# Kernel optimization log

Measured on AMD Instinct MI355X. Metric: run time of the kernel, lower is better.

The kernel has to match this reference:

```python
import jax, jax.numpy as jnp
import numpy as np


def _diffuse(x, A):
    # x: [B,C,N,L], A: [B,V,W] -> out[b,c,v,l] = sum_w x[b,c,w,l] * A[b,v,w]
    return jnp.einsum('ncwl,nvw->ncvl', x, A)


def setup_inputs() -> dict:
    key = jax.random.key(0)
    kx, k0, k1, k2, kw = jax.random.split(key, 5)
    B, C, N, L = 32, 40, 512, 12
    C_OUT = 20
    C_CAT = 7 * C  # (order*support_len + 1) * c_in = (2*3+1)*40
    x = jax.random.normal(kx, (B, C, N, L), dtype=jnp.float32)
    def mk_support(k):
        a = jax.random.uniform(k, (B, N, N), dtype=jnp.float32)
        return a / jnp.sum(a, axis=-1, keepdims=True)  # row-normalized transition
    A0, A1, A2 = mk_support(k0), mk_support(k1), mk_support(k2)
    # Conv2d(c_cat, c_out, kernel=(1,2), dilation=2) weights, stored [c_out, c_cat, 2]
    W = jax.random.normal(kw, (C_OUT, C_CAT, 2), dtype=jnp.float32) * 0.05
    b = jnp.zeros((C_OUT,), dtype=jnp.float32)
    return {'x': x, 'A0': A0, 'A1': A1, 'A2': A2, 'W': W, 'b': b}


def reference(x, A0, A1, A2, W, b):
    # dgcn.forward (eval mode, dropout is identity): order=2, support_len=3
    out = [x]
    for A in (A0, A1, A2):
        x1 = _diffuse(x, A)
        out.append(x1)
        x2 = _diffuse(x1, A)
        out.append(x2)
    h = jnp.concatenate(out, axis=1)  # [B, 7C, N, L]
    # linear_: Conv2d kernel (1,2), dilation 2, no padding -> taps at t and t+2, L_out = L-2
    y = (jnp.einsum('ncvl,oc->novl', h[..., :-2], W[:, :, 0])
         + jnp.einsum('ncvl,oc->novl', h[..., 2:], W[:, :, 1])
         + b[None, :, None, None])
    return y
```

## Files before the change

kernel.cpp:

```cpp
#include <hip/hip_runtime.h>
#include <hip/hip_bf16.h>


typedef unsigned short u16;
typedef u16 u16x4 __attribute__((ext_vector_type(4)));
typedef u16 u16x8 __attribute__((ext_vector_type(8)));
typedef __bf16 bf16x8 __attribute__((ext_vector_type(8)));
typedef float f32x4 __attribute__((ext_vector_type(4)));

#define GLD_LDS16(g, l)  __builtin_amdgcn_global_load_lds( \
    (const __attribute__((address_space(1))) void*)(g),    \
    (__attribute__((address_space(3))) void*)(l), 16, 0, 0)

__device__ __forceinline__ u16 f2bf(float f) {
    unsigned int u = __float_as_uint(f);
    u += 0x7fffu + ((u >> 16) & 1u);
    return (u16)(u >> 16);
}
__device__ __forceinline__ float bf2f(u16 h) {
    return __uint_as_float(((unsigned int)h) << 16);
}

__global__ __launch_bounds__(256) void xpose(const float* __restrict__ x,
                                             u16* __restrict__ xq)
{
    const int t = threadIdx.x, vloc = t & 63, cg = t >> 6;
    const int v = blockIdx.x * 64 + vloc, b = blockIdx.y;

    u16 vals[12][12];
    #pragma unroll
    for (int ci = 0; ci < 12; ++ci) {
        int c = cg * 12 + ci;
        if (c < 40) {
            const float* xp = x + ((size_t)(b * 40 + c) * 512 + v) * 12;
            float4 f0 = *(const float4*)xp;
            float4 f1 = *(const float4*)(xp + 4);
            float4 f2 = *(const float4*)(xp + 8);
            vals[0][ci] = f2bf(f0.x);  vals[1][ci] = f2bf(f0.y);
            vals[2][ci] = f2bf(f0.z);  vals[3][ci] = f2bf(f0.w);
            vals[4][ci] = f2bf(f1.x);  vals[5][ci] = f2bf(f1.y);
            vals[6][ci] = f2bf(f1.z);  vals[7][ci] = f2bf(f1.w);
            vals[8][ci] = f2bf(f2.x);  vals[9][ci] = f2bf(f2.y);
            vals[10][ci] = f2bf(f2.z); vals[11][ci] = f2bf(f2.w);
        } else {
            #pragma unroll
            for (int l = 0; l < 12; ++l) vals[l][ci] = 0;
        }
    }
    #pragma unroll
    for (int l = 0; l < 12; ++l) {
        u16* dst = xq + ((size_t)(b * 12 + l) * 512 + v) * 48 + cg * 12;
        u16x4 a = { vals[l][0], vals[l][1], vals[l][2], vals[l][3] };
        u16x4 c4 = { vals[l][4], vals[l][5], vals[l][6], vals[l][7] };
        u16x4 d = { vals[l][8], vals[l][9], vals[l][10], vals[l][11] };
        *(u16x4*)(dst) = a;
        *(u16x4*)(dst + 4) = c4;
        *(u16x4*)(dst + 8) = d;
    }
}

__global__ __launch_bounds__(256) void proj_x(
    const u16* __restrict__ xq, const float* __restrict__ W,
    u16* __restrict__ P1, u16* __restrict__ P2, u16* __restrict__ proj0)
{
    __shared__ u16 sA[144 * 104];
    __shared__ u16 sB[2][2 * 64 * 48];

    const int t = threadIdx.x, lane = t & 63, wid = t >> 6;
    const int b = blockIdx.y, v0 = blockIdx.x * 64;

    for (int id = t; id < 144 * 5; id += 256) {
        int m = id / 5, c0 = (id % 5) * 8;
        u16x8 e = {}, o8 = {};
        if (m < 140) {
            int o = m % 20, sg = m / 20;
            const float* wp = W + o * 560 + sg * 80 + c0 * 2;
            float4 a = *(const float4*)wp;
            float4 bb = *(const float4*)(wp + 4);
            float4 c = *(const float4*)(wp + 8);
            float4 d = *(const float4*)(wp + 12);
            e[0] = f2bf(a.x);  o8[0] = f2bf(a.y);  e[1] = f2bf(a.z);  o8[1] = f2bf(a.w);
            e[2] = f2bf(bb.x); o8[2] = f2bf(bb.y); e[3] = f2bf(bb.z); o8[3] = f2bf(bb.w);
            e[4] = f2bf(c.x);  o8[4] = f2bf(c.y);  e[5] = f2bf(c.z);  o8[5] = f2bf(c.w);
            e[6] = f2bf(d.x);  o8[6] = f2bf(d.y);  e[7] = f2bf(d.z);  o8[7] = f2bf(d.w);
        }
        *(u16x8*)(&sA[m * 104 + c0]) = e;
        *(u16x8*)(&sA[m * 104 + 40 + c0]) = o8;
    }
    for (int id = t; id < 144 * 3; id += 256) {
        int m = id / 3, k0 = 80 + (id % 3) * 8;
        u16x8 z = {};
        *(u16x8*)(&sA[m * 104 + k0]) = z;
    }

    auto stage = [&](int l, int buf) {
        u16* dst = &sB[buf][0];
        #pragma unroll
        for (int i = 0; i < 3; ++i) {
            int op = wid * 3 + i;
            int tap = op / 6, rem = op % 6;
            const u16* src = xq + ((size_t)(b * 12 + l + 2 * tap) * 512 + v0) * 48
                             + rem * 512 + lane * 8;
            GLD_LDS16(src, dst + tap * 3072 + rem * 512);
        }
    };

    stage(0, 0);
    __syncthreads();

    const int lr = lane & 15, q = lane >> 4;
    bf16x8 af[9][3];
    #pragma unroll
    for (int mf = 0; mf < 9; ++mf)
        #pragma unroll
        for (int s = 0; s < 3; ++s)
            af[mf][s] = *(const bf16x8*)(&sA[(mf * 16 + lr) * 104 + s * 32 + q * 8]);

    const int voff = (wid * 16 + lr) * 48;
    int boff[3];
    #pragma unroll
    for (int s = 0; s < 3; ++s) {
        int k = s * 32 + q * 8;
        int tap, c;
        if (k < 40)      { tap = 0; c = k; }
        else if (k < 80) { tap = 1; c = k - 40; }
        else             { tap = 1; c = 40; }
        boff[s] = tap * 3072 + voff + c;
    }

    const int v = v0 + wid * 16 + lr;
    for (int l = 0; l < 10; ++l) {
        const int cur = l & 1;
        if (l < 9) stage(l + 1, cur ^ 1);

        const u16* bb = &sB[cur][0];
        bf16x8 xf[3];
        #pragma unroll
        for (int s = 0; s < 3; ++s) xf[s] = *(const bf16x8*)(bb + boff[s]);

        f32x4 acc[9] = {};
        #pragma unroll
        for (int s = 0; s < 3; ++s)
            #pragma unroll
            for (int mf = 0; mf < 9; ++mf)
                acc[mf] = __builtin_amdgcn_mfma_f32_16x16x32_bf16(
                    af[mf][s], xf[s], acc[mf], 0, 0, 0);

        #pragma unroll
        for (int mf = 0; mf < 9; ++mf)
            #pragma unroll
            for (int i = 0; i < 4; ++i) {
                int m = mf * 16 + q * 4 + i;
                if (m < 140) {
                    int o = m % 20, sg = m / 20;
                    float val = acc[mf][i];
                    if (sg == 0) {
                        proj0[((size_t)(b * 20 + o) * 10 + l) * 512 + v] = f2bf(val);
                    } else {
                        int s2 = (sg - 1) >> 1;
                        u16* dst = ((sg - 1) & 1) ? P2 : P1;
                        dst[((size_t)(s2 * 32 + b) * 200 + o * 10 + l) * 512 + v] = f2bf(val);
                    }
                }
            }
        __syncthreads();
    }
}

template <int EPI>
__device__ __forceinline__ void gemm_body(
    const float* __restrict__ A0, const float* __restrict__ A1, const float* __restrict__ A2,
    const u16* __restrict__ Xsrc, u16* __restrict__ Odst)
{
    __shared__ float sAf[2][64 * 32];
    __shared__ u16   sXs[2][112 * 32];

    const int bid = blockIdx.x;
    const int eid = (bid & 7) * 192 + (bid >> 3);
    const int z = eid >> 4, rem = eid & 15;
    const int vblk = (rem >> 1) * 64;
    const int colbase = (rem & 1) * 112;
    const int s = z >> 5, b = z & 31;

    const float* Af = (s == 0 ? A0 : (s == 1 ? A1 : A2)) + (size_t)b * 512 * 512;
    const u16* Xb = Xsrc + (size_t)z * 200 * 512;

    const int t = threadIdx.x;
    const int lane = t & 63, wid = t >> 6;
    const int lr = lane & 15, q = lane >> 4;
    const int kc0 = q * 2;

    auto stage = [&](int kt, int buf) {
        const int w0 = kt * 32;
        float* ab = &sAf[buf][0];
        u16*   xb = &sXs[buf][0];
        #pragma unroll
        for (int i = 0; i < 2; ++i) {
            int op  = wid * 2 + i;
            int row = op * 8 + (lane >> 3);
            int pc  = lane & 7;
            const float* src = Af + (size_t)(vblk + row) * 512 + w0 + ((pc ^ (row & 7)) << 2);
            GLD_LDS16(src, ab + op * 256);
        }
        #pragma unroll
        for (int i = 0; i < 2; ++i) {
            int op = wid + i * 4;
            if (op < 7) {
                int row = op * 16 + (lane >> 2);
                int ch  = lane & 3;
                const u16* src = Xb + (size_t)(colbase + row) * 512 + w0 + ch * 8;
                GLD_LDS16(src, xb + op * 512);
            }
        }
    };

    f32x4 acc[7] = {};

    stage(0, 0);
    __syncthreads();

    for (int kt = 0; kt < 16; ++kt) {
        const int cur = kt & 1;
        if (kt < 15) stage(kt + 1, cur ^ 1);

        bf16x8 af;
        {
            int r = wid * 16 + lr;
            const float* rb = &sAf[cur][r * 32];
            f32x4 a0 = *(const f32x4*)(rb + ((kc0 ^ (r & 7)) << 2));
            f32x4 a1 = *(const f32x4*)(rb + (((kc0 + 1) ^ (r & 7)) << 2));
            union { u16x8 u; bf16x8 bv; } cv;
            cv.u = (u16x8){ f2bf(a0[0]), f2bf(a0[1]), f2bf(a0[2]), f2bf(a0[3]),
                            f2bf(a1[0]), f2bf(a1[1]), f2bf(a1[2]), f2bf(a1[3]) };
            af = cv.bv;
        }
        #pragma unroll
        for (int cf = 0; cf < 7; ++cf) {
            bf16x8 xf = *(const bf16x8*)(&sXs[cur][(cf * 16 + lr) * 32 + q * 8]);
            acc[cf] = __builtin_amdgcn_mfma_f32_16x16x32_bf16(xf, af, acc[cf], 0, 0, 0);
        }
        __syncthreads();
    }

    u16* eb = (u16*)&sAf[0][0];
    #pragma unroll
    for (int cf = 0; cf < 7; ++cf)
        #pragma unroll
        for (int i = 0; i < 4; ++i) {
            int col = cf * 16 + q * 4 + i;
            int vl  = wid * 16 + lr;
            eb[col * 68 + vl] = f2bf(acc[cf][i]);
        }
    __syncthreads();
    u16* Oz = Odst + (size_t)z * 200 * 512;
    for (int id = t; id < 112 * 8; id += 256) {
        int col = id >> 3, ch = id & 7;
        int rg = colbase + col;
        if (rg < 200) {
            u16x8 tv = *(const u16x8*)(&eb[col * 68 + ch * 8]);
            size_t gidx = (size_t)rg * 512 + vblk + ch * 8;
            if (EPI == 0) {
                u16x8 pv = *(const u16x8*)(Oz + gidx);
                u16x8 out;
                #pragma unroll
                for (int j = 0; j < 8; ++j) out[j] = f2bf(bf2f(tv[j]) + bf2f(pv[j]));
                *(u16x8*)(Oz + gidx) = out;
            } else {
                *(u16x8*)(Oz + gidx) = tv;
            }
        }
    }
}

__global__ __launch_bounds__(256) void gemm_t(
    const float* __restrict__ A0, const float* __restrict__ A1, const float* __restrict__ A2,
    const u16* __restrict__ P2, u16* __restrict__ T)
{
    gemm_body<0>(A0, A1, A2, P2, T);
}

__global__ __launch_bounds__(256) void gemm_yp(
    const float* __restrict__ A0, const float* __restrict__ A1, const float* __restrict__ A2,
    const u16* __restrict__ T, u16* __restrict__ Ypart)
{
    gemm_body<1>(A0, A1, A2, T, Ypart);
}

__global__ __launch_bounds__(256) void reduce_y(
    const u16* __restrict__ Ypart, const u16* __restrict__ proj0,
    const float* __restrict__ bias, float* __restrict__ y)
{
    int i = blockIdx.x * 256 + threadIdx.x;
    if (i >= 32 * 20 * 512) return;
    int v = i & 511;
    int r = i >> 9;
    int o = r % 20, b = r / 20;
    float bb = bias[o];
    float* yp = y + ((size_t)r * 512 + v) * 10;
    #pragma unroll
    for (int l = 0; l < 10; ++l) {
        float sum = bb + bf2f(proj0[((size_t)r * 10 + l) * 512 + v]);
        #pragma unroll
        for (int s = 0; s < 3; ++s)
            sum += bf2f(Ypart[((size_t)(s * 32 + b) * 200 + o * 10 + l) * 512 + v]);
        yp[l] = sum;
    }
}

extern "C" void kernel_launch(void* const* d_in, const int* in_sizes, int n_in,
                              void* d_out, int out_size, void* d_ws, size_t ws_size,
                              hipStream_t stream) {
    const float* x    = (const float*)d_in[0];
    const float* A0   = (const float*)d_in[1];
    const float* A1   = (const float*)d_in[2];
    const float* A2   = (const float*)d_in[3];
    const float* W    = (const float*)d_in[4];
    const float* bias = (const float*)d_in[5];
    float* y = (float*)d_out;

    const size_t PSZ = (size_t)96 * 200 * 512;
    u16* P1 = (u16*)d_ws;
    u16* P2 = P1 + PSZ;
    u16* proj0 = P2 + PSZ;
    u16* Ypart = proj0 + (size_t)32 * 20 * 10 * 512;
    u16* xq = Ypart;

    xpose<<<dim3(8, 32), 256, 0, stream>>>(x, xq);
    proj_x<<<dim3(8, 32), 256, 0, stream>>>(xq, W, P1, P2, proj0);
    gemm_t<<<dim3(1536), 256, 0, stream>>>(A0, A1, A2, P2, P1);
    gemm_yp<<<dim3(1536), 256, 0, stream>>>(A0, A1, A2, P1, Ypart);
    reduce_y<<<dim3(1280), 256, 0, stream>>>(Ypart, proj0, bias, y);
}
```

Measured before the change: 110.5 us.

## Load GEMM operands directly from global into registers, dropping LDS staging

```diff
diff --git a/kernel.cpp b/kernel.cpp
--- a/kernel.cpp
+++ b/kernel.cpp
@@ -172,8 +172,7 @@
     const float* __restrict__ A0, const float* __restrict__ A1, const float* __restrict__ A2,
     const u16* __restrict__ Xsrc, u16* __restrict__ Odst)
 {
-    __shared__ float sAf[2][64 * 32];
-    __shared__ u16   sXs[2][112 * 32];
+    __shared__ u16 eb[112 * 68];
 
     const int bid = blockIdx.x;
     const int eid = (bid & 7) * 192 + (bid >> 3);
@@ -188,61 +187,51 @@
     const int t = threadIdx.x;
     const int lane = t & 63, wid = t >> 6;
     const int lr = lane & 15, q = lane >> 4;
-    const int kc0 = q * 2;
-
-    auto stage = [&](int kt, int buf) {
-        const int w0 = kt * 32;
-        float* ab = &sAf[buf][0];
-        u16*   xb = &sXs[buf][0];
-        #pragma unroll
-        for (int i = 0; i < 2; ++i) {
-            int op  = wid * 2 + i;
-            int row = op * 8 + (lane >> 3);
-            int pc  = lane & 7;
-            const float* src = Af + (size_t)(vblk + row) * 512 + w0 + ((pc ^ (row & 7)) << 2);
-            GLD_LDS16(src, ab + op * 256);
-        }
-        #pragma unroll
-        for (int i = 0; i < 2; ++i) {
-            int op = wid + i * 4;
-            if (op < 7) {
-                int row = op * 16 + (lane >> 2);
-                int ch  = lane & 3;
-                const u16* src = Xb + (size_t)(colbase + row) * 512 + w0 + ch * 8;
-                GLD_LDS16(src, xb + op * 512);
-            }
-        }
-    };
+
+    const float* ap = Af + (size_t)(vblk + wid * 16 + lr) * 512 + q * 8;
+    const u16*   xp = Xb + (size_t)(colbase + lr) * 512 + q * 8;
 
     f32x4 acc[7] = {};
 
-    stage(0, 0);
-    __syncthreads();
-
+    f32x4 a0c = *(const f32x4*)(ap);
+    f32x4 a1c = *(const f32x4*)(ap + 4);
+    u16x8 xc[7];
+    #pragma unroll
+    for (int cf = 0; cf < 7; ++cf)
+        xc[cf] = *(const u16x8*)(xp + cf * 8192);
+
+    #pragma unroll
     for (int kt = 0; kt < 16; ++kt) {
-        const int cur = kt & 1;
-        if (kt < 15) stage(kt + 1, cur ^ 1);
-
-        bf16x8 af;
-        {
-            int r = wid * 16 + lr;
-            const float* rb = &sAf[cur][r * 32];
-            f32x4 a0 = *(const f32x4*)(rb + ((kc0 ^ (r & 7)) << 2));
-            f32x4 a1 = *(const f32x4*)(rb + (((kc0 + 1) ^ (r & 7)) << 2));
-            union { u16x8 u; bf16x8 bv; } cv;
-            cv.u = (u16x8){ f2bf(a0[0]), f2bf(a0[1]), f2bf(a0[2]), f2bf(a0[3]),
-                            f2bf(a1[0]), f2bf(a1[1]), f2bf(a1[2]), f2bf(a1[3]) };
-            af = cv.bv;
-        }
+        f32x4 a0n, a1n;
+        u16x8 xn[7];
+        if (kt < 15) {
+            const int o = (kt + 1) * 32;
+            a0n = *(const f32x4*)(ap + o);
+            a1n = *(const f32x4*)(ap + o + 4);
+            #pragma unroll
+            for (int cf = 0; cf < 7; ++cf)
+                xn[cf] = *(const u16x8*)(xp + cf * 8192 + o);
+        }
+
+        union { u16x8 u; bf16x8 bv; } cv;
+        cv.u = (u16x8){ f2bf(a0c[0]), f2bf(a0c[1]), f2bf(a0c[2]), f2bf(a0c[3]),
+                        f2bf(a1c[0]), f2bf(a1c[1]), f2bf(a1c[2]), f2bf(a1c[3]) };
+        bf16x8 af = cv.bv;
+
         #pragma unroll
         for (int cf = 0; cf < 7; ++cf) {
-            bf16x8 xf = *(const bf16x8*)(&sXs[cur][(cf * 16 + lr) * 32 + q * 8]);
-            acc[cf] = __builtin_amdgcn_mfma_f32_16x16x32_bf16(xf, af, acc[cf], 0, 0, 0);
-        }
-        __syncthreads();
-    }
-
-    u16* eb = (u16*)&sAf[0][0];
+            union { u16x8 u; bf16x8 bv; } xv;
+            xv.u = xc[cf];
+            acc[cf] = __builtin_amdgcn_mfma_f32_16x16x32_bf16(xv.bv, af, acc[cf], 0, 0, 0);
+        }
+
+        if (kt < 15) {
+            a0c = a0n; a1c = a1n;
+            #pragma unroll
+            for (int cf = 0; cf < 7; ++cf) xc[cf] = xn[cf];
+        }
+    }
+
     #pragma unroll
     for (int cf = 0; cf < 7; ++cf)
         #pragma unroll
```

New measurement: 243.5 us. 120% more time.
